# Optimization experiments

Measured on AMD Instinct MI355X. Metric: run time of the kernel, lower is better.

## Reference

```python
import jax, jax.numpy as jnp
import numpy as np

LOSS_IDX = jnp.array([0, 1])    # loss_indices from __init__
BASIS_IDX = jnp.array([0, 1])   # dtw_mapping_basis (x, y)


def _dtw_path(cost):
    """Classic DTW DP + backtrack on cost [N, M].
    Returns padded alignment path (a, b) of length N+M-1 with validity mask.
    DP is run as an anti-diagonal wavefront scan (L = N+M-1 steps)."""
    N, M = cost.shape
    L = N + M - 1
    inf = jnp.float32(jnp.inf)
    i_idx = jnp.arange(N)

    def diag_step(carry, k):
        prev1, prev2 = carry  # diagonals k-1 and k-2, indexed by row i
        j = k - i_idx
        valid = (j >= 0) & (j < M)
        c = cost[i_idx, jnp.clip(j, 0, M - 1)]
        up = jnp.concatenate([jnp.full((1,), inf), prev1[:-1]])  # D[i-1, j]
        dg = jnp.concatenate([jnp.full((1,), inf), prev2[:-1]])  # D[i-1, j-1]
        lf = prev1                                               # D[i, j-1]
        best = jnp.minimum(jnp.minimum(up, dg), lf)
        best = jnp.where(jnp.isinf(best), jnp.float32(0.0), best)  # (0,0) seed
        cur = jnp.where(valid, c + best, inf)
        return (cur, prev1), cur

    init = (jnp.full((N,), inf), jnp.full((N,), inf))
    _, diags = jax.lax.scan(diag_step, init, jnp.arange(L))  # [L, N]: D[i,j] = diags[i+j, i]

    def getD(i, j):
        ok = (i >= 0) & (j >= 0)
        return jnp.where(ok, diags[jnp.clip(i + j, 0, L - 1), jnp.clip(i, 0, N - 1)], inf)

    def bt_step(carry, _):
        i, j, done = carry
        emit_valid = jnp.logical_not(done)
        cand = jnp.stack([getD(i - 1, j - 1), getD(i - 1, j), getD(i, j - 1)])
        m = jnp.argmin(cand)  # 0: diag, 1: up, 2: left
        ni = jnp.where(m == 2, i, i - 1)
        nj = jnp.where(m == 1, j, j - 1)
        done2 = done | ((i == 0) & (j == 0))
        ni = jnp.where(done2, 0, ni)
        nj = jnp.where(done2, 0, nj)
        return (ni, nj, done2), (i, j, emit_valid)

    init_bt = (jnp.int32(N - 1), jnp.int32(M - 1), jnp.bool_(False))
    _, (a, b, valid) = jax.lax.scan(bt_step, init_bt, None, length=L)
    return a, b, valid


def _dtw_loss_single(pred, targ, subcoef):
    # DTW alignment is computed on detached (numpy in torch) basis coords.
    p = jax.lax.stop_gradient(pred)[:, BASIS_IDX]
    t = jax.lax.stop_gradient(targ)[:, BASIS_IDX]
    # euclidean pairwise distance cost [N, M]
    cost = jnp.sqrt(jnp.sum((p[:, None, :] - t[None, :, :]) ** 2, axis=-1))
    a, b, valid = _dtw_path(cost)
    d = jnp.abs(pred[a][:, LOSS_IDX] - targ[b][:, LOSS_IDX]) * subcoef  # [L, 2]
    return jnp.sum(d * valid[:, None].astype(d.dtype))


def setup_inputs() -> dict:
    key = jax.random.key(0)
    k1, k2 = jax.random.split(key)
    B, N, M, F = 32, 1024, 1024, 4
    preds = jax.random.normal(k1, (B, N, F), dtype=jnp.float32)
    targs = jax.random.normal(k2, (B, M, F), dtype=jnp.float32)
    subcoef = jnp.ones((2,), dtype=jnp.float32)
    return {"preds": preds, "targs": targs, "subcoef": subcoef}


def reference(preds, targs, subcoef):
    per_sample = jax.vmap(_dtw_loss_single, in_axes=(0, 0, None))(preds, targs, subcoef)
    return jnp.sum(per_sample)
```

## Files before the change

kernel.cpp:

```cpp
#include <hip/hip_runtime.h>
#include <math.h>

#define BATCH 32
#define NN 1024
#define MM 1024
#define RR 4
#define CC 4
#define LANES 64
#define NWAVE 4
#define TPB (MM / 4)
#define NSUP (TPB + LANES - 1)
#define LAG 72
#define TOT (NSUP + (NWAVE - 1) * LAG)
#define DEPTH 32
#define DEC_WORDS_PER_BATCH ((NN / 4) * (MM / 4))
#define DEC_BYTES ((size_t)BATCH * DEC_WORDS_PER_BATCH * 4)
#define REQ_WS DEC_BYTES
#define LPATH (NN + MM - 1)

__global__ void init_kernel(float* out) { out[0] = 0.0f; }

__device__ inline void bt_walk4(const unsigned* __restrict__ sdec, int roff,
                                int iLow, int& i, int& j, int& n,
                                unsigned* __restrict__ path)
{
    int ri = i >> 2, jc = j >> 2;
    unsigned w = sdec[(ri - roff) * 256 + jc];
    while (true) {
        const int base = (ri - roff) * 256 + jc;
        const unsigned wl = sdec[(jc > 0)    ? base - 1   : base];
        const unsigned wu = sdec[(ri > roff) ? base - 256 : base];
        const unsigned wd = sdec[(ri > roff && jc > 0) ? base - 257 : base];
        bool done = false, susp = false;
        while (true) {
            path[n++] = ((unsigned)i << 16) | (unsigned)j;
            if ((i | j) == 0) { done = true; break; }
            const unsigned m = (w >> (((i & 3) * 4 + (j & 3)) * 2)) & 3u;
            i -= (m != 2u); j -= (m != 1u);
            if (i < iLow) { susp = true; break; }
            if ((i >> 2) != ri || (j >> 2) != jc) break;
        }
        if (done || susp) break;
        const int nri = i >> 2, njc = j >> 2;
        w = (nri == ri) ? wl : ((njc == jc) ? wu : wd);
        ri = nri; jc = njc;
    }
}

__global__ __launch_bounds__(256, 1) void dtw_fused(
    const float* __restrict__ preds, const float* __restrict__ targs,
    const float* __restrict__ subcoef, unsigned* __restrict__ dec,
    float* __restrict__ out)
{
    const int b = blockIdx.x, t = threadIdx.x;
    const int l = t & 63, w = t >> 6;
    const float INF = __builtin_inff();

    __shared__ float pxA[NN], pyA[NN], txA[MM], tyA[MM];
    __shared__ float4 ring[NWAVE - 1][DEPTH];
    __shared__ unsigned sdec[128 * 256];
    __shared__ unsigned path[LPATH + 1];
    __shared__ int sI, sJ, sN;
    __shared__ float wsum[NWAVE];

    for (int it = 0; it < NN / 256; ++it) {
        const int idx = it * 256 + t;
        const float4 p4 = ((const float4*)preds)[(size_t)b * NN + idx];
        pxA[idx] = p4.x; pyA[idx] = p4.y;
        const float4 t4 = ((const float4*)targs)[(size_t)b * MM + idx];
        txA[idx] = t4.x; tyA[idx] = t4.y;
    }
    __syncthreads();

    const int i0 = (w << 8) + (l << 2);
    const float4 px4 = ((const float4*)pxA)[i0 >> 2];
    const float4 py4 = ((const float4*)pyA)[i0 >> 2];
    const float px[RR] = {px4.x, px4.y, px4.z, px4.w};
    const float py[RR] = {py4.x, py4.y, py4.z, py4.w};
    unsigned* __restrict__ decW =
        dec + (size_t)b * DEC_WORDS_PER_BATCH + ((size_t)w << 14) + (size_t)l;

    float Dp[RR], Dbot[CC], bv[CC];
    #pragma unroll
    for (int r = 0; r < RR; ++r) Dp[r] = INF;
    #pragma unroll
    for (int c = 0; c < CC; ++c) { Dbot[c] = INF; bv[c] = INF; }
    float bndRet = (w == 0 && l == 0) ? 0.0f : INF;
    float4 gcur = make_float4(INF, INF, INF, INF);
    float4 tx4 = ((const float4*)txA)[0], ty4 = ((const float4*)tyA)[0];
    const float4* __restrict__ ringR = ring[(w > 0) ? (w - 1) : 0];

    for (int u = 0; u < TOT; ++u) {
        const int ul = u - LAG * w;
        if (l == 0) {
            const bool gb = (w > 0) && (ul >= 0) && (ul < TPB);
            bv[0] = gb ? gcur.x : INF; bv[1] = gb ? gcur.y : INF;
            bv[2] = gb ? gcur.z : INF; bv[3] = gb ? gcur.w : INF;
        }
        const bool act = (ul >= l) && (ul < l + TPB);
        if (act) {
            const float cx[CC] = {tx4.x, tx4.y, tx4.z, tx4.w};
            const float cy[CC] = {ty4.x, ty4.y, ty4.z, ty4.w};
            float cost[RR][CC];
            #pragma unroll
            for (int c = 0; c < CC; ++c)
                #pragma unroll
                for (int r = 0; r < RR; ++r) {
                    const float dx = px[r] - cx[c], dy = py[r] - cy[c];
                    cost[r][c] = __builtin_amdgcn_sqrtf(dx * dx + dy * dy);
                }
            unsigned word = 0;
            #pragma unroll
            for (int c = 0; c < CC; ++c) {
                float up = bv[c];
                float dg = (c == 0) ? bndRet : bv[c - 1];
                #pragma unroll
                for (int r = 0; r < RR; ++r) {
                    const float lf = Dp[r];
                    const unsigned m = (dg <= up && dg <= lf) ? 0u
                                     : ((up <= lf) ? 1u : 2u);
                    const float D = cost[r][c] + fminf(dg, fminf(up, lf));
                    word |= m << ((r * 4 + c) * 2);
                    dg = lf; up = D; Dp[r] = D;
                }
                Dbot[c] = up;
            }
            decW[(ul & 255) << 6] = word;
            if (l == LANES - 1 && w < NWAVE - 1)
                ring[w][ul & (DEPTH - 1)] =
                    make_float4(Dbot[0], Dbot[1], Dbot[2], Dbot[3]);
        }
        bndRet = bv[CC - 1];
        #pragma unroll
        for (int c = 0; c < CC; ++c) bv[c] = __shfl_up(Dbot[c], 1);
        const int un = ul + 1;
        if (un >= l && un < l + TPB) {
            const int jn = CC * (un - l);
            tx4 = ((const float4*)txA)[jn >> 2];
            ty4 = ((const float4*)tyA)[jn >> 2];
        }
        if (w > 0 && un >= 0 && un < TPB)
            gcur = ringR[(un + 63) & (DEPTH - 1)];
        if ((u & 7) == 7) __syncthreads();
    }

    __threadfence_block();
    __syncthreads();

    const unsigned* __restrict__ decB = dec + (size_t)b * DEC_WORDS_PER_BATCH;
    {
        const uint4* g4 = (const uint4*)(decB + 32768);
        for (int k = t; k < 8192; k += 256) {
            const uint4 v = g4[k];
            const int kb = k << 2;
            const int wv = kb >> 14;
            const int rem = kb & 16383;
            const int q = rem >> 6;
            const int lb = rem & 63;
            const unsigned wd[4] = {v.x, v.y, v.z, v.w};
            #pragma unroll
            for (int e = 0; e < 4; ++e) {
                const int ll = lb + e;
                const int row = (wv << 6) + ll;
                const int jc = (q - ll) & 255;
                sdec[(row << 8) + jc] = wd[e];
            }
        }
    }
    __syncthreads();
    if (t == 0) {
        int i = NN - 1, j = MM - 1, n = 0;
        bt_walk4(sdec, 128, 512, i, j, n, path);
        sI = i; sJ = j; sN = n;
    }
    __syncthreads();
    {
        const uint4* g4 = (const uint4*)decB;
        for (int k = t; k < 8192; k += 256) {
            const uint4 v = g4[k];
            const int kb = k << 2;
            const int wv = kb >> 14;
            const int rem = kb & 16383;
            const int q = rem >> 6;
            const int lb = rem & 63;
            const unsigned wd[4] = {v.x, v.y, v.z, v.w};
            #pragma unroll
            for (int e = 0; e < 4; ++e) {
                const int ll = lb + e;
                const int row = (wv << 6) + ll;
                const int jc = (q - ll) & 255;
                sdec[(row << 8) + jc] = wd[e];
            }
        }
    }
    __syncthreads();
    if (t == 0) {
        int i = sI, j = sJ, n = sN;
        bt_walk4(sdec, 0, 0, i, j, n, path);
        sN = n;
    }
    __syncthreads();

    const float sc0 = subcoef[0], sc1 = subcoef[1];
    const int n = sN;
    float acc = 0.0f;
    for (int p = t; p < n; p += 256) {
        const unsigned e = path[p];
        const int i = (int)(e >> 16), j = (int)(e & 0xffffu);
        acc += fabsf(pxA[i] - txA[j]) * sc0 + fabsf(pyA[i] - tyA[j]) * sc1;
    }
    #pragma unroll
    for (int o = 32; o > 0; o >>= 1) acc += __shfl_down(acc, o);
    if ((t & 63) == 0) wsum[t >> 6] = acc;
    __syncthreads();
    if (t == 0) atomicAdd(out, (wsum[0] + wsum[1]) + (wsum[2] + wsum[3]));
}

__global__ __launch_bounds__(256) void dtw_fallback(
    const float* __restrict__ preds, const float* __restrict__ targs,
    const float* __restrict__ subcoef, unsigned* __restrict__ dec,
    float* __restrict__ out)
{
    const int b = blockIdx.x;
    const int t = threadIdx.x;
    const float INF = __builtin_inff();
    __shared__ float px[NN], py[NN];
    __shared__ float txy[2 * MM];
    __shared__ float bbuf[2][256];

    for (int it = 0; it < NN / 256; ++it) {
        const int idx = it * 256 + t;
        const float4 p4 = ((const float4*)preds)[(size_t)b * NN + idx];
        px[idx] = p4.x; py[idx] = p4.y;
        const float4 t4 = ((const float4*)targs)[(size_t)b * MM + idx];
        txy[2 * idx] = t4.x; txy[2 * idx + 1] = t4.y;
    }
    bbuf[0][t] = INF; bbuf[1][t] = INF;
    __syncthreads();

    float pxr[4], pyr[4], Dp[4];
    #pragma unroll
    for (int r = 0; r < 4; ++r) {
        pxr[r] = px[4 * t + r]; pyr[r] = py[4 * t + r]; Dp[r] = INF;
    }
    float dgB = (t == 0) ? 0.0f : INF;
    unsigned packed = 0;
    unsigned* decB = dec + (size_t)b * 65536;
    for (int s = 0; s < MM + 255; ++s) {
        const int j = s - t;
        const float upB = (t == 0) ? INF : bbuf[(s + 1) & 1][t - 1];
        if (j >= 0 && j < MM) {
            const float txj = txy[2 * j], tyj = txy[2 * j + 1];
            float up = upB, dg = dgB;
            unsigned mbits = 0;
            #pragma unroll
            for (int r = 0; r < 4; ++r) {
                const float dx = pxr[r] - txj, dy = pyr[r] - tyj;
                const float c = sqrtf(dx * dx + dy * dy);
                const float lf = Dp[r];
                const unsigned m = (dg <= up && dg <= lf) ? 0u
                                 : ((up <= lf) ? 1u : 2u);
                mbits |= m << (r * 8 + (j & 3) * 2);
                const float Dc = c + fminf(up, fminf(dg, lf));
                dg = lf; up = Dc; Dp[r] = Dc;
            }
            packed |= mbits;
            if ((j & 3) == 3) { decB[(unsigned)t * 256 + (j >> 2)] = packed; packed = 0; }
            bbuf[s & 1][t] = Dp[3];
        }
        dgB = upB;
        __syncthreads();
    }
    __threadfence_block();
    __syncthreads();
    if (t == 0) {
        const float sc0 = subcoef[0], sc1 = subcoef[1];
        int i = NN - 1, jj = MM - 1;
        float loss = 0.0f;
        int ti = i >> 2, tj = jj >> 2;
        unsigned wv = decB[ti * 256 + tj];
        while (true) {
            const int tjl = (tj > 0) ? tj - 1 : 0;
            const int til = (ti > 0) ? ti - 1 : 0;
            const unsigned wl = decB[ti * 256 + tjl];
            const unsigned wu = decB[til * 256 + tj];
            const unsigned wd = decB[til * 256 + tjl];
            bool done = false;
            while (true) {
                loss += fabsf(px[i] - txy[2 * jj]) * sc0
                      + fabsf(py[i] - txy[2 * jj + 1]) * sc1;
                if ((i | jj) == 0) { done = true; break; }
                const unsigned m = (wv >> (((i & 3) * 4 + (jj & 3)) * 2)) & 3u;
                i -= (m != 2u); jj -= (m != 1u);
                if ((i >> 2) != ti || (jj >> 2) != tj) break;
            }
            if (done) break;
            const int nti = i >> 2, ntj = jj >> 2;
            wv = (nti == ti) ? wl : ((ntj == tj) ? wu : wd);
            ti = nti; tj = ntj;
        }
        atomicAdd(out, loss);
    }
}

extern "C" void kernel_launch(void* const* d_in, const int* in_sizes, int n_in,
                              void* d_out, int out_size, void* d_ws, size_t ws_size,
                              hipStream_t stream) {
    const float* preds   = (const float*)d_in[0];
    const float* targs   = (const float*)d_in[1];
    const float* subcoef = (const float*)d_in[2];
    float* out = (float*)d_out;
    unsigned* dec = (unsigned*)d_ws;

    init_kernel<<<1, 1, 0, stream>>>(out);
    if (ws_size >= REQ_WS) {
        dtw_fused<<<BATCH, 256, 0, stream>>>(preds, targs, subcoef, dec, out);
    } else {
        dtw_fallback<<<BATCH, 256, 0, stream>>>(preds, targs, subcoef, dec, out);
    }
}
```

Before: 608.9 us.

## Split DTW into 128x128 panel wavefront across many blocks with separate backtrack kernel

Replaces the one-block-per-batch fused DP with an 8x8 grid of 128x128 panels per batch. Panels are processed by anti-diagonal across 15 kernel launches, each panel handled by one 64-lane wave, and panel edges are exchanged through workspace rows and columns. A separate backtrack kernel then stages decision bits into shared memory chunk by chunk and walks the path before the loss reduction. The goal is more CUs working at once than the previous 32 blocks, at the cost of many launches, global boundary traffic, and low occupancy on the edge diagonals.

```diff
diff --git a/kernel.cpp b/kernel.cpp
--- a/kernel.cpp
+++ b/kernel.cpp
@@ -4,21 +4,192 @@
 #define BATCH 32
 #define NN 1024
 #define MM 1024
-#define RR 4
-#define CC 4
-#define LANES 64
-#define NWAVE 4
-#define TPB (MM / 4)
-#define NSUP (TPB + LANES - 1)
-#define LAG 72
-#define TOT (NSUP + (NWAVE - 1) * LAG)
-#define DEPTH 32
+#define LPATH (NN + MM - 1)
+
+#define PB 128
+#define PQ 128
+#define GB 8
+#define GH 8
+#define PAN_WORDS 1536
+#define BAT_WORDS (GB * GH * PAN_WORDS)
+#define RCPL (9 * 1024)
+#define RC_OFFW ((size_t)BATCH * BAT_WORDS)
+#define BR_OFFW (RC_OFFW + (size_t)BATCH * RCPL)
+#define WS_WORDS (BR_OFFW + (size_t)BATCH * RCPL)
+#define REQ_WS_NEW (WS_WORDS * 4)
+
 #define DEC_WORDS_PER_BATCH ((NN / 4) * (MM / 4))
-#define DEC_BYTES ((size_t)BATCH * DEC_WORDS_PER_BATCH * 4)
-#define REQ_WS DEC_BYTES
-#define LPATH (NN + MM - 1)
+#define REQ_WS ((size_t)BATCH * DEC_WORDS_PER_BATCH * 4)
 
 __global__ void init_kernel(float* out) { out[0] = 0.0f; }
+
+__global__ void init2(float* __restrict__ ws, float* __restrict__ out)
+{
+    const int b = blockIdx.x, t = threadIdx.x;
+    const float INF = __builtin_inff();
+    if (b == 0 && t == 0) out[0] = 0.0f;
+    float* rc0 = ws + RC_OFFW + (size_t)b * RCPL;
+    float* br0 = ws + BR_OFFW + (size_t)b * RCPL;
+    for (int i = t; i < 1024; i += 256) { rc0[i] = INF; br0[i] = INF; }
+}
+
+__global__ __launch_bounds__(64, 1) void dtw_panel(
+    const float* __restrict__ preds, const float* __restrict__ targs,
+    float* __restrict__ ws, const int diag)
+{
+    const int b = blockIdx.y;
+    const int r0 = (diag > GH - 1) ? diag - (GH - 1) : 0;
+    const int r = r0 + blockIdx.x;
+    const int c = diag - r;
+    const int l = threadIdx.x;
+    const float INF = __builtin_inff();
+
+    __shared__ __align__(16) float txP[260], tyP[260];
+    __shared__ __align__(16) float TL[200];
+    __shared__ __align__(16) float botL[128];
+
+    if (l < 63) { txP[l] = 0.f; tyP[l] = 0.f; }
+    txP[191 + l] = 0.f; tyP[191 + l] = 0.f;
+    if (l < 6) { txP[255 + l] = 0.f; tyP[255 + l] = 0.f; }
+    TL[128 + l] = INF; if (l < 8) TL[192 + l] = INF;
+
+    const float4* tg4 = (const float4*)targs + (size_t)b * MM + c * PQ;
+    {
+        const float4 a = tg4[l], e = tg4[64 + l];
+        txP[63 + l] = a.x;      tyP[63 + l] = a.y;
+        txP[63 + 64 + l] = e.x; tyP[63 + 64 + l] = e.y;
+    }
+    const float* browR = ws + BR_OFFW + ((size_t)b * 9 + r) * 1024 + c * PQ;
+    TL[l] = browR[l]; TL[64 + l] = browR[64 + l];
+
+    const float4* pp4 = (const float4*)preds + (size_t)b * NN + r * PB;
+    const float4 p0 = pp4[2 * l], p1 = pp4[2 * l + 1];
+    const float px0 = p0.x, py0 = p0.y, px1 = p1.x, py1 = p1.y;
+
+    const float* rc = ws + RC_OFFW + ((size_t)b * 9 + c) * 1024 + r * PB;
+    float D0 = rc[2 * l], D1 = rc[2 * l + 1];
+    const float corner = (c == 0) ? ((r == 0) ? 0.0f : INF) : browR[-1];
+    const float dg0init = (l == 0) ? corner : rc[2 * l - 1];
+
+    unsigned* __restrict__ decP = (unsigned*)ws + (size_t)b * BAT_WORDS
+                                + (size_t)(r * GH + c) * PAN_WORDS + l;
+    __syncthreads();
+
+    float txb[8], tyb[8];
+    #pragma unroll
+    for (int k = 0; k < 4; ++k) { txb[k] = txP[63 + k - l]; tyb[k] = tyP[63 + k - l]; }
+    float up0prev = INF;
+
+    for (int it = 0; it < 24; ++it) {
+        const int s0 = it * 8;
+        const float4 T4a = *(const float4*)&TL[s0];
+        const float4 T4b = *(const float4*)&TL[s0 + 4];
+        const float Tv[8] = {T4a.x, T4a.y, T4a.z, T4a.w,
+                             T4b.x, T4b.y, T4b.z, T4b.w};
+        unsigned word = 0;
+        #pragma unroll
+        for (int k = 0; k < 8; ++k) {
+            const int s = s0 + k;
+            const int jq = s - l;
+            txb[(k + 4) & 7] = txP[63 + jq + 4];
+            tyb[(k + 4) & 7] = tyP[63 + jq + 4];
+            const float sh = __shfl_up(D1, 1);
+            const float up0 = (l == 0) ? Tv[k] : sh;
+            const float dg0 = (jq == 0) ? dg0init : up0prev;
+            const float tx = txb[k], ty = tyb[k];
+            const float dx0 = px0 - tx, dy0 = py0 - ty;
+            const float c0 = __builtin_amdgcn_sqrtf(dx0 * dx0 + dy0 * dy0);
+            const float mn0 = fminf(dg0, fminf(up0, D0));
+            const float D0n = c0 + mn0;
+            const unsigned m0 = (mn0 == dg0) ? 0u : ((mn0 == up0) ? 1u : 2u);
+            const float dg1 = D0;
+            const float dx1 = px1 - tx, dy1 = py1 - ty;
+            const float c1 = __builtin_amdgcn_sqrtf(dx1 * dx1 + dy1 * dy1);
+            const float mn1 = fminf(dg1, fminf(D0n, D1));
+            const float D1n = c1 + mn1;
+            const unsigned m1 = (mn1 == dg1) ? 0u : ((mn1 == D0n) ? 1u : 2u);
+            word |= (m0 | (m1 << 2)) << (4 * k);
+            const bool act = (jq >= 0) && (jq < PQ);
+            if (act) { D0 = D0n; D1 = D1n; }
+            up0prev = up0;
+            if (l == 63 && act) botL[jq] = D1n;
+        }
+        decP[it * 64] = word;
+    }
+
+    float* rcw = ws + RC_OFFW + ((size_t)b * 9 + (c + 1)) * 1024 + r * PB;
+    rcw[2 * l] = D0; rcw[2 * l + 1] = D1;
+    __syncthreads();
+    float* brw = ws + BR_OFFW + ((size_t)b * 9 + (r + 1)) * 1024 + c * PQ;
+    brw[l] = botL[l]; brw[64 + l] = botL[64 + l];
+}
+
+__global__ __launch_bounds__(256, 1) void dtw_bt(
+    const float* __restrict__ preds, const float* __restrict__ targs,
+    const float* __restrict__ subcoef, const float* __restrict__ ws,
+    float* __restrict__ out)
+{
+    const int b = blockIdx.x, t = threadIdx.x;
+    __shared__ float pxA[NN], pyA[NN], txA[MM], tyA[MM];
+    __shared__ __align__(16) unsigned sdec[24576];
+    __shared__ unsigned path[2048];
+    __shared__ int sI, sJ, sN;
+    __shared__ float wsum[4];
+
+    for (int it = 0; it < 4; ++it) {
+        const int idx = it * 256 + t;
+        const float4 p4 = ((const float4*)preds)[(size_t)b * NN + idx];
+        pxA[idx] = p4.x; pyA[idx] = p4.y;
+        const float4 t4 = ((const float4*)targs)[(size_t)b * MM + idx];
+        txA[idx] = t4.x; tyA[idx] = t4.y;
+    }
+    if (t == 0) { sI = NN - 1; sJ = MM - 1; sN = 0; }
+
+    const unsigned* decB = (const unsigned*)ws + (size_t)b * BAT_WORDS;
+    for (int pair = 3; pair >= 0; --pair) {
+        __syncthreads();
+        const uint4* g4 = (const uint4*)(decB + (size_t)pair * 24576);
+        uint4* s4 = (uint4*)sdec;
+        for (int k = t; k < 6144; k += 256) s4[k] = g4[k];
+        __syncthreads();
+        if (t == 0) {
+            int i = sI, j = sJ, n = sN;
+            const int iLow = pair * 256;
+            if (i >= iLow) {
+                int cwidx = -1; unsigned cw = 0;
+                while (true) {
+                    path[n++] = ((unsigned)i << 16) | (unsigned)j;
+                    if ((i | j) == 0) { i = -1; break; }
+                    const int rr = i >> 7, cc = j >> 7;
+                    const int ll = (i & 127) >> 1;
+                    const int ss = ll + (j & 127);
+                    const int widx = ((rr - 2 * pair) * GH + cc) * PAN_WORDS
+                                   + (ss >> 3) * 64 + ll;
+                    if (widx != cwidx) { cw = sdec[widx]; cwidx = widx; }
+                    const unsigned m = (cw >> ((ss & 7) * 4 + (i & 1) * 2)) & 3u;
+                    i -= (m != 2u); j -= (m != 1u);
+                    if (i < iLow) break;
+                }
+            }
+            sI = i; sJ = j; sN = n;
+        }
+    }
+    __syncthreads();
+
+    const float sc0 = subcoef[0], sc1 = subcoef[1];
+    const int n = sN;
+    float acc = 0.0f;
+    for (int p = t; p < n; p += 256) {
+        const unsigned e = path[p];
+        const int i = (int)(e >> 16), j = (int)(e & 0xffffu);
+        acc += fabsf(pxA[i] - txA[j]) * sc0 + fabsf(pyA[i] - tyA[j]) * sc1;
+    }
+    #pragma unroll
+    for (int o = 32; o > 0; o >>= 1) acc += __shfl_down(acc, o);
+    if ((t & 63) == 0) wsum[t >> 6] = acc;
+    __syncthreads();
+    if (t == 0) atomicAdd(out, (wsum[0] + wsum[1]) + (wsum[2] + wsum[3]));
+}
 
 __device__ inline void bt_walk4(const unsigned* __restrict__ sdec, int roff,
                                 int iLow, int& i, int& j, int& n,
@@ -47,7 +218,17 @@
     }
 }
 
-__global__ __launch_bounds__(256, 1) void dtw_fused(
+#define RRL 4
+#define CCL 4
+#define LANES 64
+#define NWAVE 4
+#define TPBL (MM / 4)
+#define NSUP (TPBL + LANES - 1)
+#define LAG 72
+#define TOTL (NSUP + (NWAVE - 1) * LAG)
+#define DEPTH 32
+
+__global__ __launch_bounds__(256, 1) void dtw_fused_legacy(
     const float* __restrict__ preds, const float* __restrict__ targs,
     const float* __restrict__ subcoef, unsigned* __restrict__ dec,
     float* __restrict__ out)
@@ -75,47 +256,47 @@
     const int i0 = (w << 8) + (l << 2);
     const float4 px4 = ((const float4*)pxA)[i0 >> 2];
     const float4 py4 = ((const float4*)pyA)[i0 >> 2];
-    const float px[RR] = {px4.x, px4.y, px4.z, px4.w};
-    const float py[RR] = {py4.x, py4.y, py4.z, py4.w};
+    const float px[RRL] = {px4.x, px4.y, px4.z, px4.w};
+    const float py[RRL] = {py4.x, py4.y, py4.z, py4.w};
     unsigned* __restrict__ decW =
         dec + (size_t)b * DEC_WORDS_PER_BATCH + ((size_t)w << 14) + (size_t)l;
 
-    float Dp[RR], Dbot[CC], bv[CC];
+    float Dp[RRL], Dbot[CCL], bv[CCL];
     #pragma unroll
-    for (int r = 0; r < RR; ++r) Dp[r] = INF;
+    for (int r = 0; r < RRL; ++r) Dp[r] = INF;
     #pragma unroll
-    for (int c = 0; c < CC; ++c) { Dbot[c] = INF; bv[c] = INF; }
+    for (int c = 0; c < CCL; ++c) { Dbot[c] = INF; bv[c] = INF; }
     float bndRet = (w == 0 && l == 0) ? 0.0f : INF;
     float4 gcur = make_float4(INF, INF, INF, INF);
     float4 tx4 = ((const float4*)txA)[0], ty4 = ((const float4*)tyA)[0];
     const float4* __restrict__ ringR = ring[(w > 0) ? (w - 1) : 0];
 
-    for (int u = 0; u < TOT; ++u) {
+    for (int u = 0; u < TOTL; ++u) {
         const int ul = u - LAG * w;
         if (l == 0) {
-            const bool gb = (w > 0) && (ul >= 0) && (ul < TPB);
+            const bool gb = (w > 0) && (ul >= 0) && (ul < TPBL);
             bv[0] = gb ? gcur.x : INF; bv[1] = gb ? gcur.y : INF;
             bv[2] = gb ? gcur.z : INF; bv[3] = gb ? gcur.w : INF;
         }
-        const bool act = (ul >= l) && (ul < l + TPB);
+        const bool act = (ul >= l) && (ul < l + TPBL);
         if (act) {
-            const float cx[CC] = {tx4.x, tx4.y, tx4.z, tx4.w};
-            const float cy[CC] = {ty4.x, ty4.y, ty4.z, ty4.w};
-            float cost[RR][CC];
+            const float cx[CCL] = {tx4.x, tx4.y, tx4.z, tx4.w};
+            const float cy[CCL] = {ty4.x, ty4.y, ty4.z, ty4.w};
+            float cost[RRL][CCL];
             #pragma unroll
-            for (int c = 0; c < CC; ++c)
+            for (int c = 0; c < CCL; ++c)
                 #pragma unroll
-                for (int r = 0; r < RR; ++r) {
+                for (int r = 0; r < RRL; ++r) {
                     const float dx = px[r] - cx[c], dy = py[r] - cy[c];
                     cost[r][c] = __builtin_amdgcn_sqrtf(dx * dx + dy * dy);
                 }
             unsigned word = 0;
             #pragma unroll
-            for (int c = 0; c < CC; ++c) {
+            for (int c = 0; c < CCL; ++c) {
                 float up = bv[c];
                 float dg = (c == 0) ? bndRet : bv[c - 1];
                 #pragma unroll
-                for (int r = 0; r < RR; ++r) {
+                for (int r = 0; r < RRL; ++r) {
                     const float lf = Dp[r];
                     const unsigned m = (dg <= up && dg <= lf) ? 0u
                                      : ((up <= lf) ? 1u : 2u);
@@ -130,16 +311,16 @@
                 ring[w][ul & (DEPTH - 1)] =
                     make_float4(Dbot[0], Dbot[1], Dbot[2], Dbot[3]);
         }
-        bndRet = bv[CC - 1];
+        bndRet = bv[CCL - 1];
         #pragma unroll
-        for (int c = 0; c < CC; ++c) bv[c] = __shfl_up(Dbot[c], 1);
+        for (int c = 0; c < CCL; ++c) bv[c] = __shfl_up(Dbot[c], 1);
         const int un = ul + 1;
-        if (un >= l && un < l + TPB) {
-            const int jn = CC * (un - l);
+        if (un >= l && un < l + TPBL) {
+            const int jn = CCL * (un - l);
             tx4 = ((const float4*)txA)[jn >> 2];
             ty4 = ((const float4*)tyA)[jn >> 2];
         }
-        if (w > 0 && un >= 0 && un < TPB)
+        if (w > 0 && un >= 0 && un < TPBL)
             gcur = ringR[(un + 63) & (DEPTH - 1)];
         if ((u & 7) == 7) __syncthreads();
     }
@@ -310,12 +491,24 @@
     const float* targs   = (const float*)d_in[1];
     const float* subcoef = (const float*)d_in[2];
     float* out = (float*)d_out;
-    unsigned* dec = (unsigned*)d_ws;
-
-    init_kernel<<<1, 1, 0, stream>>>(out);
-    if (ws_size >= REQ_WS) {
-        dtw_fused<<<BATCH, 256, 0, stream>>>(preds, targs, subcoef, dec, out);
+
+    if (ws_size >= REQ_WS_NEW) {
+        float* wsf = (float*)d_ws;
+        init2<<<BATCH, 256, 0, stream>>>(wsf, out);
+        for (int d = 0; d < GB + GH - 1; ++d) {
+            const int r0 = (d > GH - 1) ? d - (GH - 1) : 0;
+            const int r1 = (d < GB - 1) ? d : GB - 1;
+            dim3 grid(r1 - r0 + 1, BATCH);
+            dtw_panel<<<grid, 64, 0, stream>>>(preds, targs, wsf, d);
+        }
+        dtw_bt<<<BATCH, 256, 0, stream>>>(preds, targs, subcoef, wsf, out);
+    } else if (ws_size >= REQ_WS) {
+        unsigned* dec = (unsigned*)d_ws;
+        init_kernel<<<1, 1, 0, stream>>>(out);
+        dtw_fused_legacy<<<BATCH, 256, 0, stream>>>(preds, targs, subcoef, dec, out);
     } else {
+        unsigned* dec = (unsigned*)d_ws;
+        init_kernel<<<1, 1, 0, stream>>>(out);
         dtw_fallback<<<BATCH, 256, 0, stream>>>(preds, targs, subcoef, dec, out);
     }
 }
```

New measurement: 578.5 us. -5.0%, faster.
